# Kernel optimization log

Hardware: AMD Instinct MI355X
Metric: run time of the kernel (lower is better)

The kernel has to match this reference:

```python
import jax, jax.numpy as jnp
import numpy as np

B, S, DIM = 256, 196, 768      # batch, seq_len, embed_dim
POOL, LEN, TOPK = 1024, 8, 8   # pool_size, prompt length, top_k


def _l2_normalize(x, axis):
    square_sum = jnp.sum(x * x, axis=axis, keepdims=True)
    return x * jax.lax.rsqrt(jnp.maximum(square_sum, jnp.asarray(1e-12, x.dtype)))


def setup_inputs() -> dict:
    key = jax.random.key(0)
    k1, k2, k3 = jax.random.split(key, 3)
    x_embed = jax.random.normal(k1, (B, S, DIM), dtype=jnp.float32)
    # prompt_init='uniform' -> uniform(-1, 1)
    prompt = jax.random.uniform(k2, (POOL, LEN, DIM), dtype=jnp.float32, minval=-1.0, maxval=1.0)
    prompt_key = jax.random.uniform(k3, (POOL, DIM), dtype=jnp.float32, minval=-1.0, maxval=1.0)
    return {"x_embed": x_embed, "prompt": prompt, "prompt_key": prompt_key}


def reference(x_embed, prompt, prompt_key):
    bsz = x_embed.shape[0]
    # embedding_key == 'mean'
    x_embed_mean = jnp.mean(x_embed, axis=1)                      # [B, D]
    prompt_norm = _l2_normalize(prompt_key, axis=1)               # [P, D]
    x_embed_norm = _l2_normalize(x_embed_mean, axis=1)            # [B, D]
    similarity = jnp.einsum('bd,pd->bp', x_embed_norm, prompt_norm)  # [B, P]
    _, idx = jax.lax.top_k(similarity, TOPK)                      # [B, K]
    # batchwise_prompt: consensus over the batch (unique+counts == bincount over pool)
    id_counts = jnp.zeros((POOL,), jnp.int32).at[idx.ravel()].add(1)
    _, major_prompt_id = jax.lax.top_k(id_counts, TOPK)           # [K]
    idx = jnp.broadcast_to(major_prompt_id[None, :], (bsz, TOPK)) # [B, K]
    batched_prompt = prompt[idx].reshape(bsz, TOPK * LEN, DIM)    # [B, K*L, D]
    batched_key_norm = prompt_norm[idx]                           # [B, K, D]
    reduce_sim = jnp.sum(batched_key_norm * x_embed_norm[:, None, :]) / bsz
    prompted_embedding = jnp.concatenate([batched_prompt, x_embed], axis=1)  # [B, K*L+S, D]
    return prompted_embedding, reduce_sim, similarity, idx
```

## Files before the change

kernel.cpp:

```cpp
#include <hip/hip_runtime.h>
#include <math.h>

#define B_    256
#define S_    196
#define DIM_  768
#define D4_   192
#define POOL_ 1024
#define LEN_  8
#define TOPK_ 8

#define RS_OFF     51118080L
#define SIM_OFF    51118081L
#define IDX_OFF    51380225L

#define WS_XNORM   0L
#define WS_PNORMT  196608L
#define WS_PART    983040L
#define WS_ROWIDS  2031616L
#define WS_MAJOR   2032128L

__global__ void __launch_bounds__(768) prep_kernel(
        const float4* __restrict__ x4,
        const float4* __restrict__ pk4,
        float4* __restrict__ out4,
        float4* __restrict__ xnorm4,
        float* __restrict__ pT) {
    __shared__ float4 part[768];
    __shared__ float  sred[192];
    __shared__ float  sscale;
    __shared__ float  wss[12];
    int t = threadIdx.x;
    if (blockIdx.x < B_) {
        int b = blockIdx.x;
        const float4* xr = x4 + (long)b * (S_ * D4_);
        float4* ow = out4 + ((long)b * 260 + 64) * D4_;
        float4 acc = {0.f, 0.f, 0.f, 0.f};
        #pragma unroll 7
        for (int k = 0; k < 49; ++k) {
            int i = t + k * 768;
            float4 v = xr[i];
            acc.x += v.x; acc.y += v.y; acc.z += v.z; acc.w += v.w;
            ow[i] = v;
        }
        part[t] = acc;
        __syncthreads();
        float4 m = {0.f, 0.f, 0.f, 0.f};
        if (t < 192) {
            float4 a = part[t], b1 = part[t + 192], c1 = part[t + 384], d1 = part[t + 576];
            m.x = (a.x + b1.x + c1.x + d1.x) / 196.f;
            m.y = (a.y + b1.y + c1.y + d1.y) / 196.f;
            m.z = (a.z + b1.z + c1.z + d1.z) / 196.f;
            m.w = (a.w + b1.w + c1.w + d1.w) / 196.f;
            sred[t] = m.x * m.x + m.y * m.y + m.z * m.z + m.w * m.w;
        }
        __syncthreads();
        if (t < 64) {
            float s2 = sred[t] + sred[t + 64] + sred[t + 128];
            #pragma unroll
            for (int off = 32; off > 0; off >>= 1) s2 += __shfl_xor(s2, off);
            if (t == 0) sscale = 1.0f / sqrtf(fmaxf(s2, 1e-12f));
        }
        __syncthreads();
        if (t < 192) {
            float sc = sscale;
            float4 o = {m.x * sc, m.y * sc, m.z * sc, m.w * sc};
            xnorm4[(long)b * D4_ + t] = o;
        }
    } else {
        int r0 = (blockIdx.x - B_) * 4;
        int g = t / 192, i = t % 192;
        int r = r0 + g;
        float4 v = pk4[(long)r * D4_ + i];
        float ss = v.x * v.x + v.y * v.y + v.z * v.z + v.w * v.w;
        #pragma unroll
        for (int off = 32; off > 0; off >>= 1) ss += __shfl_xor(ss, off);
        if ((t & 63) == 0) wss[t >> 6] = ss;
        __syncthreads();
        float tot = wss[3 * g] + wss[3 * g + 1] + wss[3 * g + 2];
        float sc = 1.0f / sqrtf(fmaxf(tot, 1e-12f));
        int d = i * 4;
        pT[(long)d       * POOL_ + r] = v.x * sc;
        pT[(long)(d + 1) * POOL_ + r] = v.y * sc;
        pT[(long)(d + 2) * POOL_ + r] = v.z * sc;
        pT[(long)(d + 3) * POOL_ + r] = v.w * sc;
    }
}

__global__ void __launch_bounds__(512) simpart_kernel(
        const float4* __restrict__ xnorm4,
        const float4* __restrict__ pT4,
        float4* __restrict__ part4) {
    __shared__ float4 xs4[4 * 48];
    __shared__ float4 red4[4 * 256];
    int bg = blockIdx.x;
    int dc = blockIdx.y;
    int t  = threadIdx.x;
    int p4 = t & 255;
    int ds = t >> 8;
    if (t < 192) {
        int r = t / 48, q = t % 48;
        xs4[r * 48 + q] = xnorm4[(long)(bg * 4 + r) * D4_ + dc * 48 + q];
    }
    __syncthreads();
    float4 a0 = {0,0,0,0}, a1 = {0,0,0,0}, a2 = {0,0,0,0}, a3 = {0,0,0,0};
    int qbase = ds * 24;
    const float4* pbase = pT4 + ((long)dc * 192 + ds * 96) * 256 + p4;
    #pragma unroll 2
    for (int q = 0; q < 24; ++q) {
        float4 xa = xs4[qbase + q];
        float4 xb = xs4[48 + qbase + q];
        float4 xc = xs4[96 + qbase + q];
        float4 xd = xs4[144 + qbase + q];
        const float* xaf = (const float*)&xa;
        const float* xbf = (const float*)&xb;
        const float* xcf = (const float*)&xc;
        const float* xdf = (const float*)&xd;
        #pragma unroll
        for (int j = 0; j < 4; ++j) {
            float4 w = pbase[(q * 4 + j) * 256];
            a0.x += xaf[j] * w.x; a0.y += xaf[j] * w.y; a0.z += xaf[j] * w.z; a0.w += xaf[j] * w.w;
            a1.x += xbf[j] * w.x; a1.y += xbf[j] * w.y; a1.z += xbf[j] * w.z; a1.w += xbf[j] * w.w;
            a2.x += xcf[j] * w.x; a2.y += xcf[j] * w.y; a2.z += xcf[j] * w.z; a2.w += xcf[j] * w.w;
            a3.x += xdf[j] * w.x; a3.y += xdf[j] * w.y; a3.z += xdf[j] * w.z; a3.w += xdf[j] * w.w;
        }
    }
    if (ds == 1) {
        red4[p4]       = a0;
        red4[256 + p4] = a1;
        red4[512 + p4] = a2;
        red4[768 + p4] = a3;
    }
    __syncthreads();
    if (ds == 0) {
        float4 b0 = red4[p4], b1 = red4[256 + p4], b2 = red4[512 + p4], b3 = red4[768 + p4];
        a0.x += b0.x; a0.y += b0.y; a0.z += b0.z; a0.w += b0.w;
        a1.x += b1.x; a1.y += b1.y; a1.z += b1.z; a1.w += b1.w;
        a2.x += b2.x; a2.y += b2.y; a2.z += b2.z; a2.w += b2.w;
        a3.x += b3.x; a3.y += b3.y; a3.z += b3.z; a3.w += b3.w;
        long base = ((long)dc * 256 + bg * 4) * 256 + p4;
        part4[base]       = a0;
        part4[base + 256] = a1;
        part4[base + 512] = a2;
        part4[base + 768] = a3;
    }
}

__global__ void topk_sum_kernel(const float* __restrict__ part,
                                float* __restrict__ sim,
                                int* __restrict__ row_ids) {
    int row  = blockIdx.x;
    int lane = threadIdx.x;
    float v[16];
    #pragma unroll
    for (int j = 0; j < 16; ++j) {
        int p = lane + j * 64;
        float s = part[(long)row * POOL_ + p]
                + part[(long)(256 + row) * POOL_ + p]
                + part[(long)(512 + row) * POOL_ + p]
                + part[(long)(768 + row) * POOL_ + p];
        v[j] = s;
        sim[(long)row * POOL_ + p] = s;
    }
    for (int it = 0; it < TOPK_; ++it) {
        float bv = v[0];
        int   bi = lane;
        #pragma unroll
        for (int j = 1; j < 16; ++j) {
            if (v[j] > bv) { bv = v[j]; bi = lane + j * 64; }
        }
        #pragma unroll
        for (int off = 32; off > 0; off >>= 1) {
            float ov = __shfl_xor(bv, off);
            int   oi = __shfl_xor(bi, off);
            if (ov > bv || (ov == bv && oi < bi)) { bv = ov; bi = oi; }
        }
        if ((bi & 63) == lane) v[bi >> 6] = -INFINITY;
        if (lane == 0) row_ids[row * TOPK_ + it] = bi;
    }
}

__global__ void consensus_kernel(const int* __restrict__ row_ids,
                                 const float* __restrict__ sim,
                                 int* __restrict__ major,
                                 float* __restrict__ idx_out,
                                 float* __restrict__ rs_out) {
    __shared__ int   hist[POOL_];
    __shared__ int   maj[TOPK_];
    __shared__ float red[256];
    int t = threadIdx.x;
    #pragma unroll
    for (int j = 0; j < 4; ++j) hist[t + j * 256] = 0;
    __syncthreads();
    #pragma unroll
    for (int j = 0; j < TOPK_; ++j) atomicAdd(&hist[row_ids[t * TOPK_ + j]], 1);
    __syncthreads();
    if (t < 64) {
        int lane = t;
        int v[16];
        #pragma unroll
        for (int j = 0; j < 16; ++j) v[j] = hist[lane + j * 64];
        for (int it = 0; it < TOPK_; ++it) {
            int bv = v[0];
            int bi = lane;
            #pragma unroll
            for (int j = 1; j < 16; ++j) {
                if (v[j] > bv) { bv = v[j]; bi = lane + j * 64; }
            }
            #pragma unroll
            for (int off = 32; off > 0; off >>= 1) {
                int ov = __shfl_xor(bv, off);
                int oi = __shfl_xor(bi, off);
                if (ov > bv || (ov == bv && oi < bi)) { bv = ov; bi = oi; }
            }
            if (lane == 0) { maj[it] = bi; major[it] = bi; }
            if ((bi & 63) == lane) v[bi >> 6] = -1;
        }
    }
    __syncthreads();
    for (int i = t; i < B_ * TOPK_; i += 256) idx_out[i] = (float)maj[i & 7];
    float s = 0.f;
    const float* r = sim + (long)t * POOL_;
    #pragma unroll
    for (int k = 0; k < TOPK_; ++k) s += r[maj[k]];
    red[t] = s;
    __syncthreads();
    for (int off = 128; off > 0; off >>= 1) {
        if (t < off) red[t] += red[t + off];
        __syncthreads();
    }
    if (t == 0) *rs_out = red[0] / (float)B_;
}

__global__ void gather_kernel(const float4* __restrict__ prompt4,
                              const int* __restrict__ major,
                              float4* __restrict__ out4) {
    __shared__ int maj[TOPK_];
    if (threadIdx.x < TOPK_) maj[threadIdx.x] = major[threadIdx.x];
    __syncthreads();
    const long total = (long)B_ * 64 * D4_;
    for (long g = (long)blockIdx.x * blockDim.x + threadIdx.x; g < total;
         g += (long)gridDim.x * blockDim.x) {
        int  d4 = (int)(g % D4_);
        long q  = g / D4_;
        int  kl = (int)(q & 63);
        int  b  = (int)(q >> 6);
        int  pid = maj[kl >> 3];
        int  l   = kl & 7;
        out4[((long)b * 260 + kl) * D4_ + d4] = prompt4[((long)pid * LEN_ + l) * D4_ + d4];
    }
}

extern "C" void kernel_launch(void* const* d_in, const int* in_sizes, int n_in,
                              void* d_out, int out_size, void* d_ws, size_t ws_size,
                              hipStream_t stream) {
    const float* x_embed    = (const float*)d_in[0];
    const float* prompt     = (const float*)d_in[1];
    const float* prompt_key = (const float*)d_in[2];
    float* out = (float*)d_out;
    float* ws  = (float*)d_ws;

    float* xnorm   = ws + WS_XNORM;
    float* pnormT  = ws + WS_PNORMT;
    float* partial = ws + WS_PART;
    int*   row_ids = (int*)(ws + WS_ROWIDS);
    int*   major   = (int*)(ws + WS_MAJOR);

    float* out_pe  = out;
    float* out_rs  = out + RS_OFF;
    float* out_sim = out + SIM_OFF;
    float* out_idx = out + IDX_OFF;

    prep_kernel<<<512, 768, 0, stream>>>((const float4*)x_embed,
                                         (const float4*)prompt_key,
                                         (float4*)out_pe, (float4*)xnorm, pnormT);
    dim3 sgrid(64, 4);
    simpart_kernel<<<sgrid, 512, 0, stream>>>((const float4*)xnorm,
                                              (const float4*)pnormT,
                                              (float4*)partial);
    topk_sum_kernel<<<B_, 64, 0, stream>>>(partial, out_sim, row_ids);
    consensus_kernel<<<1, 256, 0, stream>>>(row_ids, out_sim, major, out_idx, out_rs);
    gather_kernel<<<2048, 256, 0, stream>>>((const float4*)prompt, major, (float4*)out_pe);
}
```

Before: 121.6 us.

## Fuse all stages into one cooperative persistent kernel with grid syncs

Replaces the five separate launches (prep, similarity partials, top-k, consensus, gather) with a single cooperative kernel of 256 blocks × 1024 threads, using grid.sync between stages. Each block copies its batch row and computes the mean while a fourth group of waves normalizes four prompt keys. Each block then handles one batch-group/dim-chunk tile for the similarity, one row's top-k, and its own slice of the prompt gather. This removes launch gaps and the separate gather launch, but adds grid-wide barriers and a serial single-block consensus phase. It also caps parallelism at 256 blocks for the memory-bound copy and gather.

```diff
diff --git a/kernel.cpp b/kernel.cpp
--- a/kernel.cpp
+++ b/kernel.cpp
@@ -1,5 +1,8 @@
 #include <hip/hip_runtime.h>
+#include <hip/hip_cooperative_groups.h>
 #include <math.h>
+
+namespace cg = cooperative_groups;
 
 #define B_    256
 #define S_    196
@@ -19,19 +22,35 @@
 #define WS_ROWIDS  2031616L
 #define WS_MAJOR   2032128L
 
-__global__ void __launch_bounds__(768) prep_kernel(
+__global__ void __launch_bounds__(1024, 4) mega_kernel(
         const float4* __restrict__ x4,
         const float4* __restrict__ pk4,
+        const float4* __restrict__ prompt4,
         float4* __restrict__ out4,
         float4* __restrict__ xnorm4,
-        float* __restrict__ pT) {
-    __shared__ float4 part[768];
+        float*  __restrict__ pT,
+        float4* __restrict__ part4,
+        int*    __restrict__ row_ids,
+        int*    __restrict__ major,
+        float*  __restrict__ sim,
+        float*  __restrict__ idx_out,
+        float*  __restrict__ rs_out) {
+    cg::grid_group grid = cg::this_grid();
+
+    __shared__ float4 lds_part[768];
     __shared__ float  sred[192];
     __shared__ float  sscale;
-    __shared__ float  wss[12];
-    int t = threadIdx.x;
-    if (blockIdx.x < B_) {
-        int b = blockIdx.x;
+    __shared__ float4 xs4[4 * 48];
+    __shared__ float4 red4[3 * 4 * 256];
+    __shared__ int    hist[POOL_];
+    __shared__ int    majs[TOPK_];
+    __shared__ float  redc[256];
+
+    const int b = blockIdx.x;
+    const int t = threadIdx.x;
+
+    float4 m = {0.f, 0.f, 0.f, 0.f};
+    if (t < 768) {
         const float4* xr = x4 + (long)b * (S_ * D4_);
         float4* ow = out4 + ((long)b * 260 + 64) * D4_;
         float4 acc = {0.f, 0.f, 0.f, 0.f};
@@ -42,242 +61,240 @@
             acc.x += v.x; acc.y += v.y; acc.z += v.z; acc.w += v.w;
             ow[i] = v;
         }
-        part[t] = acc;
-        __syncthreads();
-        float4 m = {0.f, 0.f, 0.f, 0.f};
-        if (t < 192) {
-            float4 a = part[t], b1 = part[t + 192], c1 = part[t + 384], d1 = part[t + 576];
-            m.x = (a.x + b1.x + c1.x + d1.x) / 196.f;
-            m.y = (a.y + b1.y + c1.y + d1.y) / 196.f;
-            m.z = (a.z + b1.z + c1.z + d1.z) / 196.f;
-            m.w = (a.w + b1.w + c1.w + d1.w) / 196.f;
-            sred[t] = m.x * m.x + m.y * m.y + m.z * m.z + m.w * m.w;
-        }
-        __syncthreads();
-        if (t < 64) {
-            float s2 = sred[t] + sred[t + 64] + sred[t + 128];
-            #pragma unroll
-            for (int off = 32; off > 0; off >>= 1) s2 += __shfl_xor(s2, off);
-            if (t == 0) sscale = 1.0f / sqrtf(fmaxf(s2, 1e-12f));
-        }
-        __syncthreads();
-        if (t < 192) {
-            float sc = sscale;
-            float4 o = {m.x * sc, m.y * sc, m.z * sc, m.w * sc};
-            xnorm4[(long)b * D4_ + t] = o;
-        }
+        lds_part[t] = acc;
     } else {
-        int r0 = (blockIdx.x - B_) * 4;
-        int g = t / 192, i = t % 192;
-        int r = r0 + g;
-        float4 v = pk4[(long)r * D4_ + i];
-        float ss = v.x * v.x + v.y * v.y + v.z * v.z + v.w * v.w;
+        int w = (t - 768) >> 6, lane = t & 63;
+        int r = b * 4 + w;
+        const float4* pr = pk4 + (long)r * D4_;
+        float4 v0 = pr[lane], v1 = pr[64 + lane], v2 = pr[128 + lane];
+        float ss = v0.x*v0.x + v0.y*v0.y + v0.z*v0.z + v0.w*v0.w
+                 + v1.x*v1.x + v1.y*v1.y + v1.z*v1.z + v1.w*v1.w
+                 + v2.x*v2.x + v2.y*v2.y + v2.z*v2.z + v2.w*v2.w;
         #pragma unroll
         for (int off = 32; off > 0; off >>= 1) ss += __shfl_xor(ss, off);
-        if ((t & 63) == 0) wss[t >> 6] = ss;
-        __syncthreads();
-        float tot = wss[3 * g] + wss[3 * g + 1] + wss[3 * g + 2];
-        float sc = 1.0f / sqrtf(fmaxf(tot, 1e-12f));
-        int d = i * 4;
-        pT[(long)d       * POOL_ + r] = v.x * sc;
-        pT[(long)(d + 1) * POOL_ + r] = v.y * sc;
-        pT[(long)(d + 2) * POOL_ + r] = v.z * sc;
-        pT[(long)(d + 3) * POOL_ + r] = v.w * sc;
-    }
-}
-
-__global__ void __launch_bounds__(512) simpart_kernel(
-        const float4* __restrict__ xnorm4,
-        const float4* __restrict__ pT4,
-        float4* __restrict__ part4) {
-    __shared__ float4 xs4[4 * 48];
-    __shared__ float4 red4[4 * 256];
-    int bg = blockIdx.x;
-    int dc = blockIdx.y;
-    int t  = threadIdx.x;
-    int p4 = t & 255;
-    int ds = t >> 8;
+        float sc = 1.0f / sqrtf(fmaxf(ss, 1e-12f));
+        int d0 = 4 * lane;
+        pT[(long)(d0 + 0) * POOL_ + r] = v0.x * sc;
+        pT[(long)(d0 + 1) * POOL_ + r] = v0.y * sc;
+        pT[(long)(d0 + 2) * POOL_ + r] = v0.z * sc;
+        pT[(long)(d0 + 3) * POOL_ + r] = v0.w * sc;
+        pT[(long)(256 + d0 + 0) * POOL_ + r] = v1.x * sc;
+        pT[(long)(256 + d0 + 1) * POOL_ + r] = v1.y * sc;
+        pT[(long)(256 + d0 + 2) * POOL_ + r] = v1.z * sc;
+        pT[(long)(256 + d0 + 3) * POOL_ + r] = v1.w * sc;
+        pT[(long)(512 + d0 + 0) * POOL_ + r] = v2.x * sc;
+        pT[(long)(512 + d0 + 1) * POOL_ + r] = v2.y * sc;
+        pT[(long)(512 + d0 + 2) * POOL_ + r] = v2.z * sc;
+        pT[(long)(512 + d0 + 3) * POOL_ + r] = v2.w * sc;
+    }
+    __syncthreads();
     if (t < 192) {
-        int r = t / 48, q = t % 48;
-        xs4[r * 48 + q] = xnorm4[(long)(bg * 4 + r) * D4_ + dc * 48 + q];
-    }
-    __syncthreads();
-    float4 a0 = {0,0,0,0}, a1 = {0,0,0,0}, a2 = {0,0,0,0}, a3 = {0,0,0,0};
-    int qbase = ds * 24;
-    const float4* pbase = pT4 + ((long)dc * 192 + ds * 96) * 256 + p4;
-    #pragma unroll 2
-    for (int q = 0; q < 24; ++q) {
-        float4 xa = xs4[qbase + q];
-        float4 xb = xs4[48 + qbase + q];
-        float4 xc = xs4[96 + qbase + q];
-        float4 xd = xs4[144 + qbase + q];
-        const float* xaf = (const float*)&xa;
-        const float* xbf = (const float*)&xb;
-        const float* xcf = (const float*)&xc;
-        const float* xdf = (const float*)&xd;
-        #pragma unroll
-        for (int j = 0; j < 4; ++j) {
-            float4 w = pbase[(q * 4 + j) * 256];
-            a0.x += xaf[j] * w.x; a0.y += xaf[j] * w.y; a0.z += xaf[j] * w.z; a0.w += xaf[j] * w.w;
-            a1.x += xbf[j] * w.x; a1.y += xbf[j] * w.y; a1.z += xbf[j] * w.z; a1.w += xbf[j] * w.w;
-            a2.x += xcf[j] * w.x; a2.y += xcf[j] * w.y; a2.z += xcf[j] * w.z; a2.w += xcf[j] * w.w;
-            a3.x += xdf[j] * w.x; a3.y += xdf[j] * w.y; a3.z += xdf[j] * w.z; a3.w += xdf[j] * w.w;
-        }
-    }
-    if (ds == 1) {
-        red4[p4]       = a0;
-        red4[256 + p4] = a1;
-        red4[512 + p4] = a2;
-        red4[768 + p4] = a3;
-    }
-    __syncthreads();
-    if (ds == 0) {
-        float4 b0 = red4[p4], b1 = red4[256 + p4], b2 = red4[512 + p4], b3 = red4[768 + p4];
-        a0.x += b0.x; a0.y += b0.y; a0.z += b0.z; a0.w += b0.w;
-        a1.x += b1.x; a1.y += b1.y; a1.z += b1.z; a1.w += b1.w;
-        a2.x += b2.x; a2.y += b2.y; a2.z += b2.z; a2.w += b2.w;
-        a3.x += b3.x; a3.y += b3.y; a3.z += b3.z; a3.w += b3.w;
-        long base = ((long)dc * 256 + bg * 4) * 256 + p4;
-        part4[base]       = a0;
-        part4[base + 256] = a1;
-        part4[base + 512] = a2;
-        part4[base + 768] = a3;
-    }
-}
-
-__global__ void topk_sum_kernel(const float* __restrict__ part,
-                                float* __restrict__ sim,
-                                int* __restrict__ row_ids) {
-    int row  = blockIdx.x;
-    int lane = threadIdx.x;
-    float v[16];
-    #pragma unroll
-    for (int j = 0; j < 16; ++j) {
-        int p = lane + j * 64;
-        float s = part[(long)row * POOL_ + p]
-                + part[(long)(256 + row) * POOL_ + p]
-                + part[(long)(512 + row) * POOL_ + p]
-                + part[(long)(768 + row) * POOL_ + p];
-        v[j] = s;
-        sim[(long)row * POOL_ + p] = s;
-    }
-    for (int it = 0; it < TOPK_; ++it) {
-        float bv = v[0];
-        int   bi = lane;
-        #pragma unroll
-        for (int j = 1; j < 16; ++j) {
-            if (v[j] > bv) { bv = v[j]; bi = lane + j * 64; }
-        }
-        #pragma unroll
-        for (int off = 32; off > 0; off >>= 1) {
-            float ov = __shfl_xor(bv, off);
-            int   oi = __shfl_xor(bi, off);
-            if (ov > bv || (ov == bv && oi < bi)) { bv = ov; bi = oi; }
-        }
-        if ((bi & 63) == lane) v[bi >> 6] = -INFINITY;
-        if (lane == 0) row_ids[row * TOPK_ + it] = bi;
-    }
-}
-
-__global__ void consensus_kernel(const int* __restrict__ row_ids,
-                                 const float* __restrict__ sim,
-                                 int* __restrict__ major,
-                                 float* __restrict__ idx_out,
-                                 float* __restrict__ rs_out) {
-    __shared__ int   hist[POOL_];
-    __shared__ int   maj[TOPK_];
-    __shared__ float red[256];
-    int t = threadIdx.x;
-    #pragma unroll
-    for (int j = 0; j < 4; ++j) hist[t + j * 256] = 0;
-    __syncthreads();
-    #pragma unroll
-    for (int j = 0; j < TOPK_; ++j) atomicAdd(&hist[row_ids[t * TOPK_ + j]], 1);
+        float4 a = lds_part[t], b1 = lds_part[t + 192],
+               c1 = lds_part[t + 384], d1 = lds_part[t + 576];
+        m.x = (a.x + b1.x + c1.x + d1.x) / 196.f;
+        m.y = (a.y + b1.y + c1.y + d1.y) / 196.f;
+        m.z = (a.z + b1.z + c1.z + d1.z) / 196.f;
+        m.w = (a.w + b1.w + c1.w + d1.w) / 196.f;
+        sred[t] = m.x * m.x + m.y * m.y + m.z * m.z + m.w * m.w;
+    }
     __syncthreads();
     if (t < 64) {
-        int lane = t;
-        int v[16];
+        float s2 = sred[t] + sred[t + 64] + sred[t + 128];
         #pragma unroll
-        for (int j = 0; j < 16; ++j) v[j] = hist[lane + j * 64];
+        for (int off = 32; off > 0; off >>= 1) s2 += __shfl_xor(s2, off);
+        if (t == 0) sscale = 1.0f / sqrtf(fmaxf(s2, 1e-12f));
+    }
+    __syncthreads();
+    if (t < 192) {
+        float sc = sscale;
+        float4 o = {m.x * sc, m.y * sc, m.z * sc, m.w * sc};
+        xnorm4[(long)b * D4_ + t] = o;
+    }
+
+    grid.sync();
+
+    {
+        int bg = b >> 2, dc = b & 3;
+        int p4 = t & 255;
+        int ds = t >> 8;
+        if (t < 192) {
+            int r = t / 48, q = t % 48;
+            xs4[t] = xnorm4[(long)(bg * 4 + r) * D4_ + dc * 48 + q];
+        }
+        __syncthreads();
+        float4 a0 = {0,0,0,0}, a1 = {0,0,0,0}, a2 = {0,0,0,0}, a3 = {0,0,0,0};
+        int qbase = ds * 12;
+        const float4* pT4 = (const float4*)pT;
+        const float4* pbase = pT4 + ((long)dc * 192 + ds * 48) * 256 + p4;
+        #pragma unroll 3
+        for (int q = 0; q < 12; ++q) {
+            float4 xa = xs4[qbase + q];
+            float4 xb = xs4[48 + qbase + q];
+            float4 xc = xs4[96 + qbase + q];
+            float4 xd = xs4[144 + qbase + q];
+            const float* xaf = (const float*)&xa;
+            const float* xbf = (const float*)&xb;
+            const float* xcf = (const float*)&xc;
+            const float* xdf = (const float*)&xd;
+            #pragma unroll
+            for (int j = 0; j < 4; ++j) {
+                float4 w = pbase[(q * 4 + j) * 256];
+                a0.x += xaf[j] * w.x; a0.y += xaf[j] * w.y; a0.z += xaf[j] * w.z; a0.w += xaf[j] * w.w;
+                a1.x += xbf[j] * w.x; a1.y += xbf[j] * w.y; a1.z += xbf[j] * w.z; a1.w += xbf[j] * w.w;
+                a2.x += xcf[j] * w.x; a2.y += xcf[j] * w.y; a2.z += xcf[j] * w.z; a2.w += xcf[j] * w.w;
+                a3.x += xdf[j] * w.x; a3.y += xdf[j] * w.y; a3.z += xdf[j] * w.z; a3.w += xdf[j] * w.w;
+            }
+        }
+        if (ds > 0) {
+            int s = ds - 1;
+            red4[s * 1024 +        p4] = a0;
+            red4[s * 1024 + 256  + p4] = a1;
+            red4[s * 1024 + 512  + p4] = a2;
+            red4[s * 1024 + 768  + p4] = a3;
+        }
+        __syncthreads();
+        if (ds == 0) {
+            #pragma unroll
+            for (int s = 0; s < 3; ++s) {
+                float4 b0 = red4[s * 1024 +        p4];
+                float4 b1 = red4[s * 1024 + 256  + p4];
+                float4 b2 = red4[s * 1024 + 512  + p4];
+                float4 b3 = red4[s * 1024 + 768  + p4];
+                a0.x += b0.x; a0.y += b0.y; a0.z += b0.z; a0.w += b0.w;
+                a1.x += b1.x; a1.y += b1.y; a1.z += b1.z; a1.w += b1.w;
+                a2.x += b2.x; a2.y += b2.y; a2.z += b2.z; a2.w += b2.w;
+                a3.x += b3.x; a3.y += b3.y; a3.z += b3.z; a3.w += b3.w;
+            }
+            long base = ((long)dc * 256 + bg * 4) * 256 + p4;
+            part4[base]       = a0;
+            part4[base + 256] = a1;
+            part4[base + 512] = a2;
+            part4[base + 768] = a3;
+        }
+    }
+
+    grid.sync();
+
+    if (t < 64) {
+        const float* part = (const float*)part4;
+        int row = b, lane = t;
+        float v[16];
+        #pragma unroll
+        for (int j = 0; j < 16; ++j) {
+            int p = lane + j * 64;
+            float s = part[(long)row * POOL_ + p]
+                    + part[(long)(256 + row) * POOL_ + p]
+                    + part[(long)(512 + row) * POOL_ + p]
+                    + part[(long)(768 + row) * POOL_ + p];
+            v[j] = s;
+            sim[(long)row * POOL_ + p] = s;
+        }
         for (int it = 0; it < TOPK_; ++it) {
-            int bv = v[0];
-            int bi = lane;
+            float bv = v[0];
+            int   bi = lane;
             #pragma unroll
             for (int j = 1; j < 16; ++j) {
                 if (v[j] > bv) { bv = v[j]; bi = lane + j * 64; }
             }
             #pragma unroll
             for (int off = 32; off > 0; off >>= 1) {
-                int ov = __shfl_xor(bv, off);
-                int oi = __shfl_xor(bi, off);
+                float ov = __shfl_xor(bv, off);
+                int   oi = __shfl_xor(bi, off);
                 if (ov > bv || (ov == bv && oi < bi)) { bv = ov; bi = oi; }
             }
-            if (lane == 0) { maj[it] = bi; major[it] = bi; }
-            if ((bi & 63) == lane) v[bi >> 6] = -1;
-        }
-    }
+            if ((bi & 63) == lane) v[bi >> 6] = -INFINITY;
+            if (lane == 0) row_ids[row * TOPK_ + it] = bi;
+        }
+    }
+
+    grid.sync();
+
+    if (b == 0) {
+        hist[t] = 0;
+        __syncthreads();
+        if (t < 256) {
+            #pragma unroll
+            for (int j = 0; j < TOPK_; ++j) atomicAdd(&hist[row_ids[t * TOPK_ + j]], 1);
+        }
+        __syncthreads();
+        if (t < 64) {
+            int lane = t;
+            int v[16];
+            #pragma unroll
+            for (int j = 0; j < 16; ++j) v[j] = hist[lane + j * 64];
+            for (int it = 0; it < TOPK_; ++it) {
+                int bv = v[0];
+                int bi = lane;
+                #pragma unroll
+                for (int j = 1; j < 16; ++j) {
+                    if (v[j] > bv) { bv = v[j]; bi = lane + j * 64; }
+                }
+                #pragma unroll
+                for (int off = 32; off > 0; off >>= 1) {
+                    int ov = __shfl_xor(bv, off);
+                    int oi = __shfl_xor(bi, off);
+                    if (ov > bv || (ov == bv && oi < bi)) { bv = ov; bi = oi; }
+                }
+                if (lane == 0) { majs[it] = bi; major[it] = bi; }
+                if ((bi & 63) == lane) v[bi >> 6] = -1;
+            }
+        }
+        __syncthreads();
+        for (int i = t; i < B_ * TOPK_; i += 1024) idx_out[i] = (float)majs[i & 7];
+        if (t < 256) {
+            float s = 0.f;
+            const float* r = sim + (long)t * POOL_;
+            #pragma unroll
+            for (int k = 0; k < TOPK_; ++k) s += r[majs[k]];
+            redc[t] = s;
+        }
+        __syncthreads();
+        for (int off = 128; off > 0; off >>= 1) {
+            if (t < off) redc[t] += redc[t + off];
+            __syncthreads();
+        }
+        if (t == 0) *rs_out = redc[0] / (float)B_;
+    }
+
+    grid.sync();
+
+    if (t < TOPK_) majs[t] = major[t];
     __syncthreads();
-    for (int i = t; i < B_ * TOPK_; i += 256) idx_out[i] = (float)maj[i & 7];
-    float s = 0.f;
-    const float* r = sim + (long)t * POOL_;
-    #pragma unroll
-    for (int k = 0; k < TOPK_; ++k) s += r[maj[k]];
-    red[t] = s;
-    __syncthreads();
-    for (int off = 128; off > 0; off >>= 1) {
-        if (t < off) red[t] += red[t + off];
-        __syncthreads();
-    }
-    if (t == 0) *rs_out = red[0] / (float)B_;
-}
-
-__global__ void gather_kernel(const float4* __restrict__ prompt4,
-                              const int* __restrict__ major,
-                              float4* __restrict__ out4) {
-    __shared__ int maj[TOPK_];
-    if (threadIdx.x < TOPK_) maj[threadIdx.x] = major[threadIdx.x];
-    __syncthreads();
-    const long total = (long)B_ * 64 * D4_;
-    for (long g = (long)blockIdx.x * blockDim.x + threadIdx.x; g < total;
-         g += (long)gridDim.x * blockDim.x) {
-        int  d4 = (int)(g % D4_);
-        long q  = g / D4_;
-        int  kl = (int)(q & 63);
-        int  b  = (int)(q >> 6);
-        int  pid = maj[kl >> 3];
-        int  l   = kl & 7;
-        out4[((long)b * 260 + kl) * D4_ + d4] = prompt4[((long)pid * LEN_ + l) * D4_ + d4];
+    {
+        float4* dst = out4 + (long)b * 260 * D4_;
+        #pragma unroll 4
+        for (int k = 0; k < 12; ++k) {
+            int i = t + k * 1024;
+            int kl = i / 192;
+            int d4 = i % 192;
+            int pid = majs[kl >> 3];
+            dst[i] = prompt4[((long)pid * LEN_ + (kl & 7)) * D4_ + d4];
+        }
     }
 }
 
 extern "C" void kernel_launch(void* const* d_in, const int* in_sizes, int n_in,
                               void* d_out, int out_size, void* d_ws, size_t ws_size,
                               hipStream_t stream) {
-    const float* x_embed    = (const float*)d_in[0];
-    const float* prompt     = (const float*)d_in[1];
-    const float* prompt_key = (const float*)d_in[2];
+    const float4* x4      = (const float4*)d_in[0];
+    const float4* prompt4 = (const float4*)d_in[1];
+    const float4* pk4     = (const float4*)d_in[2];
     float* out = (float*)d_out;
     float* ws  = (float*)d_ws;
 
-    float* xnorm   = ws + WS_XNORM;
-    float* pnormT  = ws + WS_PNORMT;
-    float* partial = ws + WS_PART;
-    int*   row_ids = (int*)(ws + WS_ROWIDS);
-    int*   major   = (int*)(ws + WS_MAJOR);
-
-    float* out_pe  = out;
-    float* out_rs  = out + RS_OFF;
-    float* out_sim = out + SIM_OFF;
-    float* out_idx = out + IDX_OFF;
-
-    prep_kernel<<<512, 768, 0, stream>>>((const float4*)x_embed,
-                                         (const float4*)prompt_key,
-                                         (float4*)out_pe, (float4*)xnorm, pnormT);
-    dim3 sgrid(64, 4);
-    simpart_kernel<<<sgrid, 512, 0, stream>>>((const float4*)xnorm,
-                                              (const float4*)pnormT,
-                                              (float4*)partial);
-    topk_sum_kernel<<<B_, 64, 0, stream>>>(partial, out_sim, row_ids);
-    consensus_kernel<<<1, 256, 0, stream>>>(row_ids, out_sim, major, out_idx, out_rs);
-    gather_kernel<<<2048, 256, 0, stream>>>((const float4*)prompt, major, (float4*)out_pe);
+    float4* out4    = (float4*)out;
+    float4* xnorm4  = (float4*)(ws + WS_XNORM);
+    float*  pT      = ws + WS_PNORMT;
+    float4* part4   = (float4*)(ws + WS_PART);
+    int*    row_ids = (int*)(ws + WS_ROWIDS);
+    int*    major   = (int*)(ws + WS_MAJOR);
+    float*  out_rs  = out + RS_OFF;
+    float*  out_sim = out + SIM_OFF;
+    float*  out_idx = out + IDX_OFF;
+
+    void* args[] = { (void*)&x4, (void*)&pk4, (void*)&prompt4, (void*)&out4,
+                     (void*)&xnorm4, (void*)&pT, (void*)&part4, (void*)&row_ids,
+                     (void*)&major, (void*)&out_sim, (void*)&out_idx, (void*)&out_rs };
+    hipLaunchCooperativeKernel((const void*)mega_kernel, dim3(256), dim3(1024),
+                               args, 0, stream);
 }
```

Result: slower. 237.0 us (+95.0%).

## Compute full similarity per block and fuse top-k with consensus via last-block atomic

Applied to the files above, without the earlier changes.

The similarity kernel now reduces the full 768-dim dot product inside each block, with 8 wave-slices reduced through shared memory. Blocks are split over pool chunks instead of dim chunks, so sim is written directly and the partial buffer and its re-summation pass disappear. The per-row top-k and the single-block consensus kernel are merged into one launch, where the last finishing block, found through a global atomic counter reset in prep, builds the histogram and reduce_sim. This removes one kernel launch and the partial-sum traffic, at the cost of a serialized tail block and a heavier shared-memory reduction.

```diff
diff --git a/kernel.cpp b/kernel.cpp
--- a/kernel.cpp
+++ b/kernel.cpp
@@ -15,21 +15,23 @@
 
 #define WS_XNORM   0L
 #define WS_PNORMT  196608L
-#define WS_PART    983040L
-#define WS_ROWIDS  2031616L
-#define WS_MAJOR   2032128L
+#define WS_ROWIDS  983040L
+#define WS_MAJOR   985088L
+#define WS_ROOT    985096L
 
 __global__ void __launch_bounds__(768) prep_kernel(
         const float4* __restrict__ x4,
         const float4* __restrict__ pk4,
         float4* __restrict__ out4,
         float4* __restrict__ xnorm4,
-        float* __restrict__ pT) {
+        float* __restrict__ pT,
+        int* __restrict__ root) {
     __shared__ float4 part[768];
     __shared__ float  sred[192];
     __shared__ float  sscale;
     __shared__ float  wss[12];
     int t = threadIdx.x;
+    if (blockIdx.x == 0 && t == 0) *root = 0;
     if (blockIdx.x < B_) {
         int b = blockIdx.x;
         const float4* xr = x4 + (long)b * (S_ * D4_);
@@ -86,31 +88,34 @@
     }
 }
 
-__global__ void __launch_bounds__(512) simpart_kernel(
+__global__ void __launch_bounds__(512) sim_kernel(
         const float4* __restrict__ xnorm4,
         const float4* __restrict__ pT4,
-        float4* __restrict__ part4) {
-    __shared__ float4 xs4[4 * 48];
-    __shared__ float4 red4[4 * 256];
+        float4* __restrict__ sim4) {
+    __shared__ float4 xs4[768];
+    __shared__ float4 red4[7 * 256];
     int bg = blockIdx.x;
-    int dc = blockIdx.y;
+    int pc = blockIdx.y;
     int t  = threadIdx.x;
-    int p4 = t & 255;
-    int ds = t >> 8;
-    if (t < 192) {
-        int r = t / 48, q = t % 48;
-        xs4[r * 48 + q] = xnorm4[(long)(bg * 4 + r) * D4_ + dc * 48 + q];
+    int q64 = t & 63;
+    int ds  = t >> 6;
+    {
+        int i = t;
+        xs4[i] = xnorm4[(long)(bg * 4 + i / 192) * D4_ + (i % 192)];
+        i = t + 512;
+        if (i < 768)
+            xs4[i] = xnorm4[(long)(bg * 4 + i / 192) * D4_ + (i % 192)];
     }
     __syncthreads();
     float4 a0 = {0,0,0,0}, a1 = {0,0,0,0}, a2 = {0,0,0,0}, a3 = {0,0,0,0};
-    int qbase = ds * 24;
-    const float4* pbase = pT4 + ((long)dc * 192 + ds * 96) * 256 + p4;
-    #pragma unroll 2
+    const float4* pbase = pT4 + ((long)ds * 96) * 256 + pc * 64 + q64;
+    int xq = ds * 24;
+    #pragma unroll 3
     for (int q = 0; q < 24; ++q) {
-        float4 xa = xs4[qbase + q];
-        float4 xb = xs4[48 + qbase + q];
-        float4 xc = xs4[96 + qbase + q];
-        float4 xd = xs4[144 + qbase + q];
+        float4 xa = xs4[xq + q];
+        float4 xb = xs4[192 + xq + q];
+        float4 xc = xs4[384 + xq + q];
+        float4 xd = xs4[576 + xq + q];
         const float* xaf = (const float*)&xa;
         const float* xbf = (const float*)&xb;
         const float* xcf = (const float*)&xc;
@@ -124,78 +129,87 @@
             a3.x += xdf[j] * w.x; a3.y += xdf[j] * w.y; a3.z += xdf[j] * w.z; a3.w += xdf[j] * w.w;
         }
     }
-    if (ds == 1) {
-        red4[p4]       = a0;
-        red4[256 + p4] = a1;
-        red4[512 + p4] = a2;
-        red4[768 + p4] = a3;
+    if (ds > 0) {
+        int s = ds - 1;
+        red4[s * 256 +        q64] = a0;
+        red4[s * 256 +  64  + q64] = a1;
+        red4[s * 256 + 128  + q64] = a2;
+        red4[s * 256 + 192  + q64] = a3;
     }
     __syncthreads();
     if (ds == 0) {
-        float4 b0 = red4[p4], b1 = red4[256 + p4], b2 = red4[512 + p4], b3 = red4[768 + p4];
-        a0.x += b0.x; a0.y += b0.y; a0.z += b0.z; a0.w += b0.w;
-        a1.x += b1.x; a1.y += b1.y; a1.z += b1.z; a1.w += b1.w;
-        a2.x += b2.x; a2.y += b2.y; a2.z += b2.z; a2.w += b2.w;
-        a3.x += b3.x; a3.y += b3.y; a3.z += b3.z; a3.w += b3.w;
-        long base = ((long)dc * 256 + bg * 4) * 256 + p4;
-        part4[base]       = a0;
-        part4[base + 256] = a1;
-        part4[base + 512] = a2;
-        part4[base + 768] = a3;
-    }
-}
-
-__global__ void topk_sum_kernel(const float* __restrict__ part,
-                                float* __restrict__ sim,
-                                int* __restrict__ row_ids) {
+        #pragma unroll
+        for (int s = 0; s < 7; ++s) {
+            float4 b0 = red4[s * 256 +       q64];
+            float4 b1 = red4[s * 256 +  64 + q64];
+            float4 b2 = red4[s * 256 + 128 + q64];
+            float4 b3 = red4[s * 256 + 192 + q64];
+            a0.x += b0.x; a0.y += b0.y; a0.z += b0.z; a0.w += b0.w;
+            a1.x += b1.x; a1.y += b1.y; a1.z += b1.z; a1.w += b1.w;
+            a2.x += b2.x; a2.y += b2.y; a2.z += b2.z; a2.w += b2.w;
+            a3.x += b3.x; a3.y += b3.y; a3.z += b3.z; a3.w += b3.w;
+        }
+        long base = ((long)(bg * 4)) * 256 + pc * 64 + q64;
+        sim4[base]           = a0;
+        sim4[base + 256]     = a1;
+        sim4[base + 512]     = a2;
+        sim4[base + 768]     = a3;
+    }
+}
+
+__global__ void __launch_bounds__(64) topk_consensus_kernel(
+        const float* __restrict__ sim,
+        int*   __restrict__ row_ids,
+        int*   __restrict__ major,
+        float* __restrict__ idx_out,
+        float* __restrict__ rs_out,
+        int*   __restrict__ root) {
+    __shared__ int hist[POOL_];
+    __shared__ int majs[TOPK_];
+    __shared__ int lastFlag;
     int row  = blockIdx.x;
     int lane = threadIdx.x;
-    float v[16];
-    #pragma unroll
-    for (int j = 0; j < 16; ++j) {
-        int p = lane + j * 64;
-        float s = part[(long)row * POOL_ + p]
-                + part[(long)(256 + row) * POOL_ + p]
-                + part[(long)(512 + row) * POOL_ + p]
-                + part[(long)(768 + row) * POOL_ + p];
-        v[j] = s;
-        sim[(long)row * POOL_ + p] = s;
-    }
-    for (int it = 0; it < TOPK_; ++it) {
-        float bv = v[0];
-        int   bi = lane;
-        #pragma unroll
-        for (int j = 1; j < 16; ++j) {
-            if (v[j] > bv) { bv = v[j]; bi = lane + j * 64; }
-        }
-        #pragma unroll
-        for (int off = 32; off > 0; off >>= 1) {
-            float ov = __shfl_xor(bv, off);
-            int   oi = __shfl_xor(bi, off);
-            if (ov > bv || (ov == bv && oi < bi)) { bv = ov; bi = oi; }
-        }
-        if ((bi & 63) == lane) v[bi >> 6] = -INFINITY;
-        if (lane == 0) row_ids[row * TOPK_ + it] = bi;
-    }
-}
-
-__global__ void consensus_kernel(const int* __restrict__ row_ids,
-                                 const float* __restrict__ sim,
-                                 int* __restrict__ major,
-                                 float* __restrict__ idx_out,
-                                 float* __restrict__ rs_out) {
-    __shared__ int   hist[POOL_];
-    __shared__ int   maj[TOPK_];
-    __shared__ float red[256];
-    int t = threadIdx.x;
-    #pragma unroll
-    for (int j = 0; j < 4; ++j) hist[t + j * 256] = 0;
-    __syncthreads();
-    #pragma unroll
-    for (int j = 0; j < TOPK_; ++j) atomicAdd(&hist[row_ids[t * TOPK_ + j]], 1);
-    __syncthreads();
-    if (t < 64) {
-        int lane = t;
+    {
+        float v[16];
+        const float* r = sim + (long)row * POOL_;
+        #pragma unroll
+        for (int j = 0; j < 16; ++j) v[j] = r[lane + j * 64];
+        for (int it = 0; it < TOPK_; ++it) {
+            float bv = v[0];
+            int   bi = lane;
+            #pragma unroll
+            for (int j = 1; j < 16; ++j) {
+                if (v[j] > bv) { bv = v[j]; bi = lane + j * 64; }
+            }
+            #pragma unroll
+            for (int off = 32; off > 0; off >>= 1) {
+                float ov = __shfl_xor(bv, off);
+                int   oi = __shfl_xor(bi, off);
+                if (ov > bv || (ov == bv && oi < bi)) { bv = ov; bi = oi; }
+            }
+            if ((bi & 63) == lane) v[bi >> 6] = -INFINITY;
+            if (lane == 0) row_ids[row * TOPK_ + it] = bi;
+        }
+    }
+    if (lane == 0) {
+        int prev = __hip_atomic_fetch_add(root, 1, __ATOMIC_ACQ_REL,
+                                          __HIP_MEMORY_SCOPE_SYSTEM);
+        lastFlag = (prev == B_ - 1);
+    }
+    __syncthreads();
+    if (!lastFlag) return;
+
+    #pragma unroll
+    for (int j = 0; j < 16; ++j) hist[lane + j * 64] = 0;
+    __syncthreads();
+    #pragma unroll
+    for (int rr = 0; rr < 4; ++rr) {
+        int r = lane + rr * 64;
+        #pragma unroll
+        for (int j = 0; j < TOPK_; ++j) atomicAdd(&hist[row_ids[r * TOPK_ + j]], 1);
+    }
+    __syncthreads();
+    {
         int v[16];
         #pragma unroll
         for (int j = 0; j < 16; ++j) v[j] = hist[lane + j * 64];
@@ -212,23 +226,26 @@
                 int oi = __shfl_xor(bi, off);
                 if (ov > bv || (ov == bv && oi < bi)) { bv = ov; bi = oi; }
             }
-            if (lane == 0) { maj[it] = bi; major[it] = bi; }
+            if (lane == 0) { majs[it] = bi; major[it] = bi; }
             if ((bi & 63) == lane) v[bi >> 6] = -1;
         }
     }
     __syncthreads();
-    for (int i = t; i < B_ * TOPK_; i += 256) idx_out[i] = (float)maj[i & 7];
+    #pragma unroll
+    for (int k = 0; k < 32; ++k) {
+        int i = lane + k * 64;
+        idx_out[i] = (float)majs[i & 7];
+    }
     float s = 0.f;
-    const float* r = sim + (long)t * POOL_;
-    #pragma unroll
-    for (int k = 0; k < TOPK_; ++k) s += r[maj[k]];
-    red[t] = s;
-    __syncthreads();
-    for (int off = 128; off > 0; off >>= 1) {
-        if (t < off) red[t] += red[t + off];
-        __syncthreads();
-    }
-    if (t == 0) *rs_out = red[0] / (float)B_;
+    #pragma unroll
+    for (int rr = 0; rr < 4; ++rr) {
+        const float* r = sim + (long)(lane + rr * 64) * POOL_;
+        #pragma unroll
+        for (int k = 0; k < TOPK_; ++k) s += r[majs[k]];
+    }
+    #pragma unroll
+    for (int off = 32; off > 0; off >>= 1) s += __shfl_xor(s, off);
+    if (lane == 0) *rs_out = s / (float)B_;
 }
 
 __global__ void gather_kernel(const float4* __restrict__ prompt4,
@@ -253,31 +270,26 @@
 extern "C" void kernel_launch(void* const* d_in, const int* in_sizes, int n_in,
                               void* d_out, int out_size, void* d_ws, size_t ws_size,
                               hipStream_t stream) {
-    const float* x_embed    = (const float*)d_in[0];
-    const float* prompt     = (const float*)d_in[1];
-    const float* prompt_key = (const float*)d_in[2];
+    const float4* x4      = (const float4*)d_in[0];
+    const float4* prompt4 = (const float4*)d_in[1];
+    const float4* pk4     = (const float4*)d_in[2];
     float* out = (float*)d_out;
     float* ws  = (float*)d_ws;
 
-    float* xnorm   = ws + WS_XNORM;
-    float* pnormT  = ws + WS_PNORMT;
-    float* partial = ws + WS_PART;
-    int*   row_ids = (int*)(ws + WS_ROWIDS);
-    int*   major   = (int*)(ws + WS_MAJOR);
-
-    float* out_pe  = out;
-    float* out_rs  = out + RS_OFF;
-    float* out_sim = out + SIM_OFF;
-    float* out_idx = out + IDX_OFF;
-
-    prep_kernel<<<512, 768, 0, stream>>>((const float4*)x_embed,
-                                         (const float4*)prompt_key,
-                                         (float4*)out_pe, (float4*)xnorm, pnormT);
-    dim3 sgrid(64, 4);
-    simpart_kernel<<<sgrid, 512, 0, stream>>>((const float4*)xnorm,
-                                              (const float4*)pnormT,
-                                              (float4*)partial);
-    topk_sum_kernel<<<B_, 64, 0, stream>>>(partial, out_sim, row_ids);
-    consensus_kernel<<<1, 256, 0, stream>>>(row_ids, out_sim, major, out_idx, out_rs);
-    gather_kernel<<<2048, 256, 0, stream>>>((const float4*)prompt, major, (float4*)out_pe);
-}
+    float4* out4    = (float4*)out;
+    float4* xnorm4  = (float4*)(ws + WS_XNORM);
+    float*  pT      = ws + WS_PNORMT;
+    int*    row_ids = (int*)(ws + WS_ROWIDS);
+    int*    major   = (int*)(ws + WS_MAJOR);
+    int*    root    = (int*)(ws + WS_ROOT);
+    float*  out_rs  = out + RS_OFF;
+    float*  out_sim = out + SIM_OFF;
+    float*  out_idx = out + IDX_OFF;
+
+    prep_kernel<<<512, 768, 0, stream>>>(x4, pk4, out4, xnorm4, pT, root);
+    dim3 sg(64, 4);
+    sim_kernel<<<sg, 512, 0, stream>>>(xnorm4, (const float4*)pT, (float4*)out_sim);
+    topk_consensus_kernel<<<B_, 64, 0, stream>>>(out_sim, row_ids, major,
+                                                 out_idx, out_rs, root);
+    gather_kernel<<<2048, 256, 0, stream>>>(prompt4, major, out4);
+}
```

Result: slower. 129.2 us (+6.3%).
